# Optimization experiments

Measured on AMD Instinct MI355X. Metric: run time of the kernel, lower is better.

The kernel has to match this reference:

```python
import jax, jax.numpy as jnp
import numpy as np

R = 8
EPS = 1e-08
EPSS = 1e-12


def _diff_x(x, r):
    left = x[:, :, r:2 * r + 1]
    middle = x[:, :, 2 * r + 1:] - x[:, :, :-2 * r - 1]
    right = x[:, :, -1:] - x[:, :, -2 * r - 1:-r - 1]
    return jnp.concatenate([left, middle, right], axis=2)


def _diff_y(x, r):
    left = x[:, :, :, r:2 * r + 1]
    middle = x[:, :, :, 2 * r + 1:] - x[:, :, :, :-2 * r - 1]
    right = x[:, :, :, -1:] - x[:, :, :, -2 * r - 1:-r - 1]
    return jnp.concatenate([left, middle, right], axis=3)


def box_filter(x, r):
    # cumsum-based (2r+1)x(2r+1) box sum with clamped borders (matches torch BoxFilter)
    return _diff_y(jnp.cumsum(_diff_x(jnp.cumsum(x, axis=2), r), axis=3), r)


def bilinear_resize(x, H, W):
    # F.interpolate(mode='bilinear', align_corners=True) for NCHW
    n, c, h, w = x.shape
    ys = jnp.linspace(0.0, h - 1.0, H)
    xs = jnp.linspace(0.0, w - 1.0, W)
    y0 = jnp.floor(ys).astype(jnp.int32)
    x0 = jnp.floor(xs).astype(jnp.int32)
    y1 = jnp.minimum(y0 + 1, h - 1)
    x1 = jnp.minimum(x0 + 1, w - 1)
    wy = (ys - y0).astype(x.dtype)[None, None, :, None]
    wx = (xs - x0).astype(x.dtype)[None, None, None, :]
    rows = jnp.take(x, y0, axis=2) * (1.0 - wy) + jnp.take(x, y1, axis=2) * wy
    return jnp.take(rows, x0, axis=3) * (1.0 - wx) + jnp.take(rows, x1, axis=3) * wx


def setup_inputs() -> dict:
    key = jax.random.key(0)
    k1, k2, k3, k4 = jax.random.split(key, 4)
    return {
        "lr_x": jax.random.normal(k1, (4, 3, 256, 256), dtype=jnp.float32),
        "lr_y": jax.random.normal(k2, (4, 3, 256, 256), dtype=jnp.float32),
        "hr_x": jax.random.normal(k3, (4, 3, 1024, 1024), dtype=jnp.float32),
        "l_a": jax.random.uniform(k4, (4, 3, 256, 256), dtype=jnp.float32),
    }


def reference(lr_x, lr_y, hr_x, l_a):
    n, c, h, w = lr_x.shape
    _, _, hh, wh = hr_x.shape
    dt = lr_x.dtype

    N = box_filter(jnp.ones((1, 1, h, w), dtype=dt), R)  # local window counts

    l_a = jnp.abs(l_a) + EPSS
    l_t = l_a / jnp.sum(l_a)

    mean_a = box_filter(l_a) if False else box_filter(l_a, R) / N
    mean_a2xy = box_filter(l_a * l_a * lr_x * lr_y, R) / N
    mean_tax = box_filter(l_t * l_a * lr_x, R) / N
    mean_ay = box_filter(l_a * lr_y, R) / N
    mean_a2x2 = box_filter(l_a * l_a * lr_x * lr_x, R) / N
    mean_ax = box_filter(l_a * lr_x, R) / N

    temp = jnp.abs(mean_a2x2 - N * mean_tax * mean_ax)
    A = (mean_a2xy - N * mean_tax * mean_ay) / (temp + EPS)
    b = (mean_ay - A * mean_ax) / mean_a

    A = box_filter(A, R) / N
    b = box_filter(b, R) / N

    mean_A = bilinear_resize(A, hh, wh)
    mean_b = bilinear_resize(b, hh, wh)
    return (mean_A * hr_x + mean_b).astype(jnp.float32)
```

## Files before the change

kernel.cpp:

```cpp
#include <hip/hip_runtime.h>


#define RAD 8
#define HH 256
#define WW 256
#define NC 12
#define PS (HH*WW)
#define SCALE (255.0f/1023.0f)

#define NA2 36
#define NC2 20
#define AP2 37
#define HP2 21

__device__ __forceinline__ int swz3072(int b) { return (b & 7) * 384 + (b >> 3); }
__device__ __forceinline__ int swz1152(int b) { return (b & 7) * 144 + (b >> 3); }

__device__ __forceinline__ float run17(float x) {
    float s = x + __shfl_up(x, 1, 64);
    s += __shfl_up(s, 2, 64);
    s += __shfl_up(s, 4, 64);
    s += __shfl_up(s, 8, 64);
    s += __shfl_up(x, 16, 64);
    return s;
}

__global__ __launch_bounds__(256) void k_reduce(const float* __restrict__ la,
                                                float* __restrict__ partials) {
    int tid = threadIdx.x;
    __shared__ float ls[4];
    const float4* p4 = (const float4*)la;
    int base = blockIdx.x * 2048 + tid;
    float s = 0.f;
    #pragma unroll
    for (int i = 0; i < 8; i++) {
        float4 v = p4[base + i * 256];
        s += (fabsf(v.x) + 1e-12f) + (fabsf(v.y) + 1e-12f) +
             (fabsf(v.z) + 1e-12f) + (fabsf(v.w) + 1e-12f);
    }
    for (int off = 32; off > 0; off >>= 1) s += __shfl_down(s, off, 64);
    int lane = tid & 63, wid = tid >> 6;
    if (lane == 0) ls[wid] = s;
    __syncthreads();
    if (tid == 0) partials[blockIdx.x] = ls[0] + ls[1] + ls[2] + ls[3];
}

__global__ __launch_bounds__(256) void k_ab(const float* __restrict__ la,
                                            const float* __restrict__ lx,
                                            const float* __restrict__ ly,
                                            const float* __restrict__ partials,
                                            float* __restrict__ Ab,
                                            float* __restrict__ Bb) {
    int tid = threadIdx.x, lane = tid & 63, wv = tid >> 6;
    int gw = swz1152(blockIdx.x) * 4 + wv;
    int p  = gw / 384;
    int r  = gw - p * 384;
    int s  = r >> 6;
    int bd = r & 63;
    int i0 = bd << 2;
    int C0 = s * 48;
    int col = C0 - 8 + lane;
    bool vc = (col >= 0) && (col < WW);
    int colc = min(max(col, 0), WW - 1);
    const float* pa = la + p * PS + colc;
    const float* px = lx + p * PS + colc;
    const float* py = ly + p * PS + colc;

    float psum = partials[lane] + ((lane < 32) ? partials[lane + 64] : 0.0f);
    #pragma unroll
    for (int off = 32; off > 0; off >>= 1) psum += __shfl_xor(psum, off, 64);
    float invS = 1.0f / psum;

    int  cA  = C0 - 16 + lane;
    bool vcA = (lane >= 16) && (cA < WW);
    float cxA = (float)(min(cA + RAD, WW - 1) - max(cA - RAD, 0) + 1);

    float s0 = 0, s1 = 0, s2 = 0, s3 = 0, s4 = 0, s5 = 0;
    auto accum = [&](int rr, float sg) {
        float va = 0.f, vx = 0.f, vy = 0.f;
        if (vc) { int o = rr * WW; va = pa[o]; vx = px[o]; vy = py[o]; }
        float a  = vc ? (fabsf(va) + 1e-12f) : 0.f;
        float ax = a * vx, ay = a * vy;
        s0 = fmaf(sg, a, s0); s1 = fmaf(sg, ax, s1); s2 = fmaf(sg, ay, s2);
        s3 = fmaf(sg, a * ax, s3); s4 = fmaf(sg, ax * ax, s4); s5 = fmaf(sg, ax * ay, s5);
    };

    #pragma unroll
    for (int d = -8; d <= 8; ++d) {
        int rr = i0 + d;
        if (rr >= 0 && rr < HH) accum(rr, 1.0f);
    }

    float* Apl = Ab + p * PS;
    float* Bpl = Bb + p * PS;
    #pragma unroll
    for (int k = 0; k < 4; ++k) {
        int m = i0 + k;
        if (k > 0) {
            int ra = m + 8; if (ra < HH) accum(ra, 1.0f);
            int rs = m - 9; if (rs >= 0) accum(rs, -1.0f);
        }
        float h0 = run17(s0), h1 = run17(s1), h2 = run17(s2),
              h3 = run17(s3), h4 = run17(s4), h5 = run17(s5);
        float cy = (float)(min(m + RAD, HH - 1) - max(m - RAD, 0) + 1);
        float Nv = cxA * cy, invN = 1.0f / Nv;
        float m_a = h0 * invN, m_ax = h1 * invN, m_ay = h2 * invN;
        float m_tax = h3 * invN * invS;
        float m_a2x2 = h4 * invN, m_a2xy = h5 * invN;
        float tempv = fabsf(m_a2x2 - Nv * m_tax * m_ax);
        float Av = (m_a2xy - Nv * m_tax * m_ay) / (tempv + 1e-8f);
        float bv = (m_ay - Av * m_ax) / m_a;
        if (vcA) {
            int o = m * WW + cA;
            Apl[o] = Av;
            Bpl[o] = bv;
        }
    }
}

__global__ __launch_bounds__(256) void k_tile(const float* __restrict__ Ab,
                                              const float* __restrict__ Bb,
                                              const float* __restrict__ hrx,
                                              float* __restrict__ out) {
    __shared__ float sA[NA2 * AP2], sB[NA2 * AP2];
    __shared__ float sHA[NA2 * HP2], sHB[NA2 * HP2];
    float* mAb = sA;
    float* mBb = sB;

    int tid = threadIdx.x;
    int b  = swz3072(blockIdx.x);
    int p  = b >> 8;
    int t  = b & 255;
    int ti = t >> 4, tj = t & 15;
    int I0 = ti << 6, J0 = tj << 6;
    int Lr0 = max(0, (I0 * 255) / 1023 - 1);
    int Lc0 = max(0, (J0 * 255) / 1023 - 1);

    const float* Apl = Ab + p * PS;
    const float* Bpl = Bb + p * PS;
    for (int idx = tid; idx < NA2 * NA2; idx += 256) {
        int r = idx / NA2, c = idx - r * NA2;
        int gr = Lr0 - 8 + r, gc = Lc0 - 8 + c;
        float av = 0.f, bv = 0.f;
        if (gr >= 0 && gr < HH && gc >= 0 && gc < WW) {
            int o = gr * WW + gc;
            av = Apl[o]; bv = Bpl[o];
        }
        sA[r * AP2 + c] = av;
        sB[r * AP2 + c] = bv;
    }
    __syncthreads();

    for (int job = tid; job < 2 * NA2 * NC2; job += 256) {
        int which = (job >= NA2 * NC2);
        int rest  = which ? job - NA2 * NC2 : job;
        int r = rest / NC2, c = rest - r * NC2;
        const float* rp = (which ? sB : sA) + r * AP2 + c;
        float s = 0.f;
        #pragma unroll
        for (int j = 0; j < 17; ++j) s += rp[j];
        (which ? sHB : sHA)[r * HP2 + c] = s;
    }
    __syncthreads();

    for (int job = tid; job < 2 * NC2 * NC2; job += 256) {
        int which = (job >= NC2 * NC2);
        int rest  = which ? job - NC2 * NC2 : job;
        int r = rest / NC2, c = rest - r * NC2;
        const float* sp = (which ? sHB : sHA) + r * HP2 + c;
        float s = 0.f;
        #pragma unroll
        for (int j = 0; j < 17; ++j) s += sp[j * HP2];
        int gj = Lc0 + c, gi = Lr0 + r;
        float cxw = (float)(min(gj + RAD, WW - 1) - max(gj - RAD, 0) + 1);
        float cyw = (float)(min(gi + RAD, HH - 1) - max(gi - RAD, 0) + 1);
        (which ? mBb : mAb)[r * HP2 + c] = s / (cxw * cyw);
    }
    __syncthreads();

    {
        int col4 = tid & 15;
        int rg   = tid >> 4;
        int J4 = (J0 >> 2) + col4;
        int Jp = J4 << 2;
        int xb = (int)((float)Jp * SCALE);
        int i1 = min(xb + 1, WW - 1), i2 = min(xb + 2, WW - 1);
        int lxb = xb - Lc0, li1 = i1 - Lc0, li2 = i2 - Lc0;
        float wxv[4]; bool hs[4];
        #pragma unroll
        for (int k = 0; k < 4; k++) {
            float xsk = (float)(Jp + k) * SCALE;
            int x0 = (int)xsk;
            wxv[k] = xsk - (float)x0;
            hs[k] = (x0 > xb);
        }
        const float4* h4 = (const float4*)hrx;
        float4* o4 = (float4*)out;
        int planeHR = p * 262144;

        int hidx0 = planeHR + (I0 + 0 * 16 + rg) * 256 + J4;
        int hidx1 = planeHR + (I0 + 1 * 16 + rg) * 256 + J4;
        int hidx2 = planeHR + (I0 + 2 * 16 + rg) * 256 + J4;
        int hidx3 = planeHR + (I0 + 3 * 16 + rg) * 256 + J4;
        float4 hp0 = h4[hidx0], hp1 = h4[hidx1], hp2 = h4[hidx2], hp3 = h4[hidx3];

        #pragma unroll
        for (int it = 0; it < 4; ++it) {
            int row = (it << 4) + rg;
            int I = I0 + row;
            float ysf = (float)I * SCALE;
            int y0 = (int)ysf;
            float wy = ysf - (float)y0;
            int y1 = min(y0 + 1, HH - 1);
            int ly0 = y0 - Lr0, ly1 = y1 - Lr0;
            const float* a0p = mAb + ly0 * HP2;
            const float* a1p = mAb + ly1 * HP2;
            const float* b0p = mBb + ly0 * HP2;
            const float* b1p = mBb + ly1 * HP2;
            float A0a = a0p[lxb], A0b = a0p[li1], A0c = a0p[li2];
            float A1a = a1p[lxb], A1b = a1p[li1], A1c = a1p[li2];
            float B0a = b0p[lxb], B0b = b0p[li1], B0c = b0p[li2];
            float B1a = b1p[lxb], B1b = b1p[li1], B1c = b1p[li2];
            float4 h = (it == 0) ? hp0 : (it == 1) ? hp1 : (it == 2) ? hp2 : hp3;
            int hidx = (it == 0) ? hidx0 : (it == 1) ? hidx1 : (it == 2) ? hidx2 : hidx3;
            float hv[4] = {h.x, h.y, h.z, h.w};
            float ov[4];
            float omwy = 1.0f - wy;
            #pragma unroll
            for (int k = 0; k < 4; k++) {
                bool hb = hs[k];
                float Alo0 = hb ? A0b : A0a, Ahi0 = hb ? A0c : A0b;
                float Alo1 = hb ? A1b : A1a, Ahi1 = hb ? A1c : A1b;
                float Blo0 = hb ? B0b : B0a, Bhi0 = hb ? B0c : B0b;
                float Blo1 = hb ? B1b : B1a, Bhi1 = hb ? B1c : B1b;
                float wx = wxv[k], omwx = 1.0f - wx;
                float Ar0 = Alo0 * omwx + Ahi0 * wx;
                float Ar1 = Alo1 * omwx + Ahi1 * wx;
                float Br0 = Blo0 * omwx + Bhi0 * wx;
                float Br1 = Blo1 * omwx + Bhi1 * wx;
                float Avv = Ar0 * omwy + Ar1 * wy;
                float Bvv = Br0 * omwy + Br1 * wy;
                ov[k] = Avv * hv[k] + Bvv;
            }
            float4 o; o.x = ov[0]; o.y = ov[1]; o.z = ov[2]; o.w = ov[3];
            o4[hidx] = o;
        }
    }
}

extern "C" void kernel_launch(void* const* d_in, const int* in_sizes, int n_in,
                              void* d_out, int out_size, void* d_ws, size_t ws_size,
                              hipStream_t stream) {
    const float* lr_x = (const float*)d_in[0];
    const float* lr_y = (const float*)d_in[1];
    const float* hr_x = (const float*)d_in[2];
    const float* l_a  = (const float*)d_in[3];
    float* out = (float*)d_out;

    float* ws       = (float*)d_ws;
    float* partials = ws;
    float* Ab       = ws + 256;
    float* Bb       = Ab + NC * PS;

    k_reduce<<<96, 256, 0, stream>>>(l_a, partials);
    k_ab    <<<1152, 256, 0, stream>>>(l_a, lr_x, lr_y, partials, Ab, Bb);
    k_tile  <<<3072, 256, 0, stream>>>(Ab, Bb, hr_x, out);
}
```

Baseline: 138.1 us.

## Fuse A/b coefficient computation into the upsampling tile kernel

Removes the separate k_ab kernel and the global A/b intermediate buffers. Each k_tile block now computes its own 36x36 halo of A and b coefficients from l_a, lr_x and lr_y straight into shared memory, with each of the 4 waves producing 9 rows. This drops one kernel launch and the write/read round trip of the A/b planes. In exchange it recomputes overlapping halos across neighbouring tiles, because 3072 blocks each redo their 36x36 region plus a 16-column, 17-row stencil apron.

Measured after the change: 161.4 us. 16.9% more time.

```diff
diff --git a/kernel.cpp b/kernel.cpp
--- a/kernel.cpp
+++ b/kernel.cpp
@@ -1,5 +1,4 @@
 #include <hip/hip_runtime.h>
-
 
 #define RAD 8
 #define HH 256
@@ -14,7 +13,6 @@
 #define HP2 21
 
 __device__ __forceinline__ int swz3072(int b) { return (b & 7) * 384 + (b >> 3); }
-__device__ __forceinline__ int swz1152(int b) { return (b & 7) * 144 + (b >> 3); }
 
 __device__ __forceinline__ float run17(float x) {
     float s = x + __shfl_up(x, 1, 64);
@@ -45,89 +43,18 @@
     if (tid == 0) partials[blockIdx.x] = ls[0] + ls[1] + ls[2] + ls[3];
 }
 
-__global__ __launch_bounds__(256) void k_ab(const float* __restrict__ la,
-                                            const float* __restrict__ lx,
-                                            const float* __restrict__ ly,
-                                            const float* __restrict__ partials,
-                                            float* __restrict__ Ab,
-                                            float* __restrict__ Bb) {
-    int tid = threadIdx.x, lane = tid & 63, wv = tid >> 6;
-    int gw = swz1152(blockIdx.x) * 4 + wv;
-    int p  = gw / 384;
-    int r  = gw - p * 384;
-    int s  = r >> 6;
-    int bd = r & 63;
-    int i0 = bd << 2;
-    int C0 = s * 48;
-    int col = C0 - 8 + lane;
-    bool vc = (col >= 0) && (col < WW);
-    int colc = min(max(col, 0), WW - 1);
-    const float* pa = la + p * PS + colc;
-    const float* px = lx + p * PS + colc;
-    const float* py = ly + p * PS + colc;
-
-    float psum = partials[lane] + ((lane < 32) ? partials[lane + 64] : 0.0f);
-    #pragma unroll
-    for (int off = 32; off > 0; off >>= 1) psum += __shfl_xor(psum, off, 64);
-    float invS = 1.0f / psum;
-
-    int  cA  = C0 - 16 + lane;
-    bool vcA = (lane >= 16) && (cA < WW);
-    float cxA = (float)(min(cA + RAD, WW - 1) - max(cA - RAD, 0) + 1);
-
-    float s0 = 0, s1 = 0, s2 = 0, s3 = 0, s4 = 0, s5 = 0;
-    auto accum = [&](int rr, float sg) {
-        float va = 0.f, vx = 0.f, vy = 0.f;
-        if (vc) { int o = rr * WW; va = pa[o]; vx = px[o]; vy = py[o]; }
-        float a  = vc ? (fabsf(va) + 1e-12f) : 0.f;
-        float ax = a * vx, ay = a * vy;
-        s0 = fmaf(sg, a, s0); s1 = fmaf(sg, ax, s1); s2 = fmaf(sg, ay, s2);
-        s3 = fmaf(sg, a * ax, s3); s4 = fmaf(sg, ax * ax, s4); s5 = fmaf(sg, ax * ay, s5);
-    };
-
-    #pragma unroll
-    for (int d = -8; d <= 8; ++d) {
-        int rr = i0 + d;
-        if (rr >= 0 && rr < HH) accum(rr, 1.0f);
-    }
-
-    float* Apl = Ab + p * PS;
-    float* Bpl = Bb + p * PS;
-    #pragma unroll
-    for (int k = 0; k < 4; ++k) {
-        int m = i0 + k;
-        if (k > 0) {
-            int ra = m + 8; if (ra < HH) accum(ra, 1.0f);
-            int rs = m - 9; if (rs >= 0) accum(rs, -1.0f);
-        }
-        float h0 = run17(s0), h1 = run17(s1), h2 = run17(s2),
-              h3 = run17(s3), h4 = run17(s4), h5 = run17(s5);
-        float cy = (float)(min(m + RAD, HH - 1) - max(m - RAD, 0) + 1);
-        float Nv = cxA * cy, invN = 1.0f / Nv;
-        float m_a = h0 * invN, m_ax = h1 * invN, m_ay = h2 * invN;
-        float m_tax = h3 * invN * invS;
-        float m_a2x2 = h4 * invN, m_a2xy = h5 * invN;
-        float tempv = fabsf(m_a2x2 - Nv * m_tax * m_ax);
-        float Av = (m_a2xy - Nv * m_tax * m_ay) / (tempv + 1e-8f);
-        float bv = (m_ay - Av * m_ax) / m_a;
-        if (vcA) {
-            int o = m * WW + cA;
-            Apl[o] = Av;
-            Bpl[o] = bv;
-        }
-    }
-}
-
-__global__ __launch_bounds__(256) void k_tile(const float* __restrict__ Ab,
-                                              const float* __restrict__ Bb,
+__global__ __launch_bounds__(256) void k_tile(const float* __restrict__ la,
+                                              const float* __restrict__ lx,
+                                              const float* __restrict__ ly,
                                               const float* __restrict__ hrx,
+                                              const float* __restrict__ partials,
                                               float* __restrict__ out) {
     __shared__ float sA[NA2 * AP2], sB[NA2 * AP2];
     __shared__ float sHA[NA2 * HP2], sHB[NA2 * HP2];
     float* mAb = sA;
     float* mBb = sB;
 
-    int tid = threadIdx.x;
+    int tid = threadIdx.x, lane = tid & 63, wv = tid >> 6;
     int b  = swz3072(blockIdx.x);
     int p  = b >> 8;
     int t  = b & 255;
@@ -136,18 +63,69 @@
     int Lr0 = max(0, (I0 * 255) / 1023 - 1);
     int Lc0 = max(0, (J0 * 255) / 1023 - 1);
 
-    const float* Apl = Ab + p * PS;
-    const float* Bpl = Bb + p * PS;
-    for (int idx = tid; idx < NA2 * NA2; idx += 256) {
-        int r = idx / NA2, c = idx - r * NA2;
-        int gr = Lr0 - 8 + r, gc = Lc0 - 8 + c;
-        float av = 0.f, bv = 0.f;
-        if (gr >= 0 && gr < HH && gc >= 0 && gc < WW) {
-            int o = gr * WW + gc;
-            av = Apl[o]; bv = Bpl[o];
-        }
-        sA[r * AP2 + c] = av;
-        sB[r * AP2 + c] = bv;
+    float psum = partials[lane] + ((lane < 32) ? partials[lane + 64] : 0.0f);
+    #pragma unroll
+    for (int off = 32; off > 0; off >>= 1) psum += __shfl_xor(psum, off, 64);
+    float invS = 1.0f / psum;
+
+    {
+        int C0  = Lc0 - 8;
+        int col = C0 - 8 + lane;
+        bool vc = (col >= 0) && (col < WW);
+        int colc = min(max(col, 0), WW - 1);
+        const float* pa = la + p * PS + colc;
+        const float* px = lx + p * PS + colc;
+        const float* py = ly + p * PS + colc;
+
+        int  cA    = C0 - 16 + lane;
+        int  cIdx  = lane - 16;
+        bool vLane = (lane >= 16) && (lane < 16 + NA2);
+        bool vcA   = (cA >= 0) && (cA < WW);
+        float cxA  = (float)(min(cA + RAD, WW - 1) - max(cA - RAD, 0) + 1);
+
+        float s0 = 0, s1 = 0, s2 = 0, s3 = 0, s4 = 0, s5 = 0;
+        auto accum = [&](int rr, float sg) {
+            float va = 0.f, vx = 0.f, vy = 0.f;
+            if (vc) { int o = rr * WW; va = pa[o]; vx = px[o]; vy = py[o]; }
+            float a  = vc ? (fabsf(va) + 1e-12f) : 0.f;
+            float ax = a * vx, ay = a * vy;
+            s0 = fmaf(sg, a, s0); s1 = fmaf(sg, ax, s1); s2 = fmaf(sg, ay, s2);
+            s3 = fmaf(sg, a * ax, s3); s4 = fmaf(sg, ax * ax, s4); s5 = fmaf(sg, ax * ay, s5);
+        };
+
+        int R0 = Lr0 - 8 + 9 * wv;
+        #pragma unroll
+        for (int d = -8; d <= 8; ++d) {
+            int rr = R0 + d;
+            if (rr >= 0 && rr < HH) accum(rr, 1.0f);
+        }
+        #pragma unroll
+        for (int k = 0; k < 9; ++k) {
+            int m = R0 + k;
+            if (k > 0) {
+                int ra = m + 8; if (ra >= 0 && ra < HH) accum(ra, 1.0f);
+                int rs = m - 9; if (rs >= 0 && rs < HH) accum(rs, -1.0f);
+            }
+            float h0 = run17(s0), h1 = run17(s1), h2 = run17(s2),
+                  h3 = run17(s3), h4 = run17(s4), h5 = run17(s5);
+            float Av = 0.f, bv = 0.f;
+            if (m >= 0 && m < HH) {
+                float cy = (float)(min(m + RAD, HH - 1) - max(m - RAD, 0) + 1);
+                float Nv = cxA * cy, invN = 1.0f / Nv;
+                float m_a = h0 * invN, m_ax = h1 * invN, m_ay = h2 * invN;
+                float m_tax = h3 * invN * invS;
+                float m_a2x2 = h4 * invN, m_a2xy = h5 * invN;
+                float tempv = fabsf(m_a2x2 - Nv * m_tax * m_ax);
+                float Avt = (m_a2xy - Nv * m_tax * m_ay) / (tempv + 1e-8f);
+                float bvt = (m_ay - Avt * m_ax) / m_a;
+                if (vcA) { Av = Avt; bv = bvt; }
+            }
+            if (vLane) {
+                int rIdx = 9 * wv + k;
+                sA[rIdx * AP2 + cIdx] = Av;
+                sB[rIdx * AP2 + cIdx] = bv;
+            }
+        }
     }
     __syncthreads();
 
@@ -256,13 +234,8 @@
     const float* hr_x = (const float*)d_in[2];
     const float* l_a  = (const float*)d_in[3];
     float* out = (float*)d_out;
-
-    float* ws       = (float*)d_ws;
-    float* partials = ws;
-    float* Ab       = ws + 256;
-    float* Bb       = Ab + NC * PS;
+    float* partials = (float*)d_ws;
 
     k_reduce<<<96, 256, 0, stream>>>(l_a, partials);
-    k_ab    <<<1152, 256, 0, stream>>>(l_a, lr_x, lr_y, partials, Ab, Bb);
-    k_tile  <<<3072, 256, 0, stream>>>(Ab, Bb, hr_x, out);
-}
+    k_tile  <<<3072, 256, 0, stream>>>(l_a, lr_x, lr_y, hr_x, partials, out);
+}
```
